# Kernel tuning notes

Hardware: AMD Instinct MI355X
Metric: run time of the kernel (lower is better)

Reference implementation:

```python
import jax, jax.numpy as jnp
import numpy as np

B, N, D, H, HID, EN = 2, 4096, 128, 4, 32, 16
ALPHA = 0.2           # LeakyReLU slope
NEG = -9e15           # masked_fill value from the original code


def setup_inputs() -> dict:
    key = jax.random.key(0)
    ks = jax.random.split(key, 6)
    fea = jax.random.normal(ks[0], (B, N, D), dtype=jnp.float32)
    # binary dense adjacency (regulon x gene), square here so narrow() is identity
    adj = jax.random.randint(ks[1], (B, N, N), 0, 2).astype(jnp.float32)
    # per-head GAT params (xavier-ish scale)
    W_heads = jax.random.normal(ks[2], (H, D, HID), dtype=jnp.float32) * 0.1
    a_heads = jax.random.normal(ks[3], (H, 2 * HID, 1), dtype=jnp.float32) * 0.1
    W_last = jax.random.normal(ks[4], (H * HID, EN), dtype=jnp.float32) * 0.1
    a_last = jax.random.normal(ks[5], (2 * EN, 1), dtype=jnp.float32) * 0.1
    return {"fea_mats": fea, "adj_mats": adj, "W_heads": W_heads,
            "a_heads": a_heads, "W_last": W_last, "a_last": a_last}


def _gat_layer(x, adj, W, a, concat):
    # x: [N, d_in], adj: [nr, N], W: [d_in, out], a: [2*out, 1]
    out_dim = W.shape[1]
    wh = x @ W                                   # [N, out]
    nr = adj.shape[0]
    wh1 = wh[:nr] @ a[:out_dim]                  # [nr, 1]
    wh2 = wh @ a[out_dim:]                       # [N, 1]
    e = jax.nn.leaky_relu(wh1 + wh2.T, ALPHA)    # [nr, N]
    # _prepare_attentions: mask by adj, weight by adj, fill zeros with -9e15
    att = jnp.where(adj != 0, e * adj, 0.0)
    att = jnp.where(att == 0, NEG, att)
    att = jax.nn.softmax(att, axis=1)
    # the original detaches attention via a numpy roundtrip
    att = jax.lax.stop_gradient(att)
    res = att @ wh                               # [nr, out]
    return jax.nn.elu(res) if concat else res


def reference(fea_mats, adj_mats, W_heads, a_heads, W_last, a_last):
    def per_sample(x, adj):
        # multi-head attention layers (concat=True), vmapped over heads
        heads = jax.vmap(lambda W, a: _gat_layer(x, adj, W, a, True))(W_heads, a_heads)  # [H, N, HID]
        xcat = jnp.transpose(heads, (1, 0, 2)).reshape(x.shape[0], H * HID)  # torch.cat(dim=1)
        nr = adj.shape[0]
        out = _gat_layer(xcat, adj[:, :nr], W_last, a_last, False)  # adj.narrow(1,0,nr)
        return jax.nn.elu(out)  # [N, EN]
    return jax.vmap(per_sample)(fea_mats, adj_mats)  # [B, N, EN]
```

## Files before the change

### kernel.cpp

```cpp
#include <hip/hip_runtime.h>
#include <hip/hip_bf16.h>
#include <stdint.h>

#define B_ 2
#define N_ 4096
#define D_ 128
#define H_ 4
#define HID_ 32
#define EN_ 16
#define ALPHA_ 0.2f
#define S1_ 4
#define S2_ 4
#define LOG2E_ 1.4426950408889634f

typedef __attribute__((ext_vector_type(8))) short bf16x8;
typedef __attribute__((ext_vector_type(4))) float f32x4;
typedef __attribute__((ext_vector_type(8))) unsigned short u16x8;

__device__ __forceinline__ float bf2f(unsigned short u) {
    return __uint_as_float(((unsigned int)u) << 16);
}
__device__ __forceinline__ unsigned short f2bf_rne(float x) {
    unsigned int u = __float_as_uint(x);
    unsigned int r = ((u >> 16) & 1u) + 0x7fffu;
    return (unsigned short)((u + r) >> 16);
}
__device__ __forceinline__ unsigned int f2key(float x) {
    unsigned int u = __float_as_uint(x);
    return (u & 0x80000000u) ? ~u : (u | 0x80000000u);
}
__device__ __forceinline__ float key2f(unsigned int k) {
    unsigned int u = (k & 0x80000000u) ? (k ^ 0x80000000u) : ~k;
    return __uint_as_float(u);
}

__global__ __launch_bounds__(256) void proj1_kernel(
    const float* __restrict__ fea, const float* __restrict__ Wh,
    float* __restrict__ wh)
{
    __shared__ float Ws[D_ * HID_];
    __shared__ float xs[8][D_];
    const int b = blockIdx.z, h = blockIdx.y;
    const int i0 = blockIdx.x * 8;
    const int tid = threadIdx.x;
    const float* Wp = Wh + h * D_ * HID_;
    for (int idx = tid * 4; idx < D_ * HID_; idx += 1024)
        *(float4*)&Ws[idx] = *(const float4*)(Wp + idx);
    const float* xp = fea + ((size_t)b * N_ + i0) * D_;
    *(float4*)&xs[(tid * 4) >> 7][(tid * 4) & 127] = *(const float4*)(xp + tid * 4);
    __syncthreads();
    const int r = tid >> 5, d = tid & 31;
    float acc = 0.f;
#pragma unroll 8
    for (int k = 0; k < D_; ++k) acc += xs[r][k] * Ws[k * HID_ + d];
    wh[(((size_t)b * H_ + h) * N_ + i0 + r) * HID_ + d] = acc;
}

__global__ __launch_bounds__(128) void proj1b_kernel(
    const float* __restrict__ wh, const float* __restrict__ a_heads,
    float* __restrict__ wh1, float* __restrict__ wh2,
    unsigned int* __restrict__ mkey, unsigned short* __restrict__ whTt)
{
    __shared__ float as_[2 * HID_];
    __shared__ unsigned short ts[32][136];
    const int b = blockIdx.z, h = blockIdx.y, tid = threadIdx.x;
    const int i = blockIdx.x * 128 + tid;
    if (tid < 2 * HID_) as_[tid] = a_heads[h * 2 * HID_ + tid];
    __syncthreads();
    const float* row = wh + (((size_t)b * H_ + h) * N_ + i) * HID_;
    float rv[32];
#pragma unroll
    for (int q = 0; q < 8; ++q) *(float4*)&rv[q * 4] = ((const float4*)row)[q];
    float a1 = 0.f, a2 = 0.f;
#pragma unroll
    for (int d = 0; d < HID_; ++d) {
        float v = rv[d];
        a1 += v * as_[d]; a2 += v * as_[HID_ + d];
        ts[d][tid] = f2bf_rne(v);
    }
    a1 *= LOG2E_; a2 *= LOG2E_;
    const size_t o = (size_t)(b * H_ + h) * N_ + i;
    wh1[o] = a1; wh2[o] = a2;
    float m = a2;
#pragma unroll
    for (int off = 32; off; off >>= 1) m = fmaxf(m, __shfl_xor(m, off));
    if ((tid & 63) == 0) atomicMax(&mkey[b * H_ + h], f2key(m));
    __syncthreads();
    const size_t base = ((size_t)(b * H_ + h) * 64 + blockIdx.x * 2) * 2048;
#pragma unroll
    for (int r = 0; r < 4; ++r) {
        int l = r * 128 + tid;
        int jb = l >> 8, d = (l >> 3) & 31, part = l & 7;
        *(u16x8*)(whTt + base + (size_t)jb * 2048 + d * 64 + part * 8) =
            *(const u16x8*)&ts[d][jb * 64 + part * 8];
    }
}

__global__ __launch_bounds__(256) void attn1_kernel(
    const float* __restrict__ adj, const unsigned short* __restrict__ whT,
    const float* __restrict__ wh1, const float* __restrict__ wh2,
    const unsigned int* __restrict__ mkey,
    float* __restrict__ x2num, float* __restrict__ l1sum)
{
    __shared__ float adj_s[2][16][68];
    const int b = blockIdx.z, split = blockIdx.y, i0 = blockIdx.x * 16;
    const int tid = threadIdx.x, lane = tid & 63, h = tid >> 6;
    const int m = lane & 15, quad = lane >> 4;
    const float w1r = wh1[(size_t)(b * H_ + h) * N_ + i0 + m];
    const float Mh = key2f(mkey[b * H_ + h]);
    const float sbound = w1r + Mh;
    const float mr = fmaxf(sbound, ALPHA_ * sbound);
    const float* adjb = adj + ((size_t)b * N_ + i0) * N_;
    const float* w2h = wh2 + (size_t)(b * H_ + h) * N_;
    const unsigned short* whTp = whT + (size_t)(b * H_ + h) * 64 * 2048;
    const int sr = tid >> 4, sc4 = (tid & 15) * 4;
    f32x4 acc0 = {0.f, 0.f, 0.f, 0.f}, acc1 = {0.f, 0.f, 0.f, 0.f};
    float lsum = 0.f;
    const int TL = N_ / S1_ / 64;
    const int jt0 = split * (N_ / S1_);

    auto stage = [&](int jt, int bufi) {
        *(float4*)&adj_s[bufi][sr][sc4] = *(const float4*)(adjb + (size_t)sr * N_ + jt + sc4);
    };
    stage(jt0, 0);
    int buf = 0;
    for (int t = 0; t < TL; ++t) {
        __syncthreads();
        if (t + 1 < TL) stage(jt0 + (t + 1) * 64, buf ^ 1);
        const int jt = jt0 + t * 64;
        const int jb = split * TL + t;
#pragma unroll
        for (int ks = 0; ks < 2; ++ks) {
            const int ko = ks * 32 + quad * 8;
            float av[8], wv8[8];
            *(float4*)&av[0] = *(const float4*)&adj_s[buf][m][ko];
            *(float4*)&av[4] = *(const float4*)&adj_s[buf][m][ko + 4];
            *(float4*)&wv8[0] = *(const float4*)(w2h + jt + ko);
            *(float4*)&wv8[4] = *(const float4*)(w2h + jt + ko + 4);
            bf16x8 af;
#pragma unroll
            for (int jj = 0; jj < 8; ++jj) {
                float s = w1r + wv8[jj];
                float e = fmaxf(s, ALPHA_ * s);
                float tt = (av[jj] == 0.f || s == 0.f) ? -__builtin_inff() : (e - mr);
                float p = __builtin_amdgcn_exp2f(tt);
                unsigned short pb = f2bf_rne(p);
                af[jj] = (short)pb;
                lsum += bf2f(pb);
            }
            const unsigned short* bp = whTp + (size_t)jb * 2048 + m * 64 + ks * 32 + quad * 8;
            bf16x8 b0 = *(const bf16x8*)bp;
            bf16x8 b1 = *(const bf16x8*)(bp + 1024);
            acc0 = __builtin_amdgcn_mfma_f32_16x16x32_bf16(af, b0, acc0, 0, 0, 0);
            acc1 = __builtin_amdgcn_mfma_f32_16x16x32_bf16(af, b1, acc1, 0, 0, 0);
        }
        buf ^= 1;
    }
#pragma unroll
    for (int reg = 0; reg < 4; ++reg) {
        int row = quad * 4 + reg;
        float* dst = x2num + ((size_t)b * N_ + i0 + row) * (H_ * HID_) + h * HID_;
        atomicAdd(dst + m, acc0[reg]);
        atomicAdd(dst + 16 + m, acc1[reg]);
    }
    lsum += __shfl_xor(lsum, 16);
    lsum += __shfl_xor(lsum, 32);
    if (quad == 0) atomicAdd(l1sum + ((size_t)b * N_ + i0 + m) * H_ + h, lsum);
}

__global__ __launch_bounds__(256) void proj2_kernel(
    const float* __restrict__ x2num, const float* __restrict__ l1sum,
    const float* __restrict__ Wl, float* __restrict__ whl2)
{
    __shared__ float Ws[D_ * EN_];
    __shared__ float xs[16][D_];
    const int b = blockIdx.y, i0 = blockIdx.x * 16, tid = threadIdx.x;
    for (int idx = tid * 4; idx < D_ * EN_; idx += 1024)
        *(float4*)&Ws[idx] = *(const float4*)(Wl + idx);
    for (int idx = tid * 4; idx < 16 * D_; idx += 1024) {
        int r = idx >> 7, hd = idx & 127, h = hd >> 5;
        const size_t i = (size_t)b * N_ + i0 + r;
        float linv = 1.f / fmaxf(l1sum[i * H_ + h], 1e-30f);
        float4 v = *(const float4*)(x2num + i * D_ + hd);
        float o0 = v.x * linv, o1 = v.y * linv, o2 = v.z * linv, o3 = v.w * linv;
        xs[r][hd]     = o0 > 0.f ? o0 : expm1f(o0);
        xs[r][hd + 1] = o1 > 0.f ? o1 : expm1f(o1);
        xs[r][hd + 2] = o2 > 0.f ? o2 : expm1f(o2);
        xs[r][hd + 3] = o3 > 0.f ? o3 : expm1f(o3);
    }
    __syncthreads();
    const int r = tid >> 4, e = tid & 15;
    float acc = 0.f;
#pragma unroll 8
    for (int k = 0; k < D_; ++k) acc += xs[r][k] * Ws[k * EN_ + e];
    whl2[((size_t)b * N_ + i0 + r) * EN_ + e] = acc;
}

__global__ __launch_bounds__(128) void proj2b_kernel(
    const float* __restrict__ whl2, const float* __restrict__ a_last,
    float* __restrict__ wh1b, float* __restrict__ wh2b,
    unsigned int* __restrict__ mkey2, unsigned short* __restrict__ whT2t)
{
    __shared__ float as_[2 * EN_];
    __shared__ unsigned short ts[16][136];
    const int b = blockIdx.y, tid = threadIdx.x;
    const int i = blockIdx.x * 128 + tid;
    if (tid < 2 * EN_) as_[tid] = a_last[tid];
    __syncthreads();
    const float* row = whl2 + ((size_t)b * N_ + i) * EN_;
    float rv[16];
#pragma unroll
    for (int q = 0; q < 4; ++q) *(float4*)&rv[q * 4] = ((const float4*)row)[q];
    float a1 = 0.f, a2 = 0.f;
#pragma unroll
    for (int e = 0; e < EN_; ++e) {
        float v = rv[e];
        a1 += v * as_[e]; a2 += v * as_[EN_ + e];
        ts[e][tid] = f2bf_rne(v);
    }
    a1 *= LOG2E_; a2 *= LOG2E_;
    wh1b[(size_t)b * N_ + i] = a1; wh2b[(size_t)b * N_ + i] = a2;
    float m = a2;
#pragma unroll
    for (int off = 32; off; off >>= 1) m = fmaxf(m, __shfl_xor(m, off));
    if ((tid & 63) == 0) atomicMax(mkey2 + b, f2key(m));
    __syncthreads();
    const size_t base = ((size_t)b * 64 + blockIdx.x * 2) * 1024;
#pragma unroll
    for (int r = 0; r < 2; ++r) {
        int l = r * 128 + tid;
        int jb = l >> 7, d = (l >> 3) & 15, part = l & 7;
        *(u16x8*)(whT2t + base + (size_t)jb * 1024 + d * 64 + part * 8) =
            *(const u16x8*)&ts[d][jb * 64 + part * 8];
    }
}

__global__ __launch_bounds__(256) void attn2_kernel(
    const float* __restrict__ adj, const unsigned short* __restrict__ whT2,
    const float* __restrict__ wh1b, const float* __restrict__ wh2b,
    const unsigned int* __restrict__ mkey2,
    float* __restrict__ out_num, float* __restrict__ out_l)
{
    __shared__ float adj_s[16][260];
    const int b = blockIdx.z, split = blockIdx.y, i0 = blockIdx.x * 16;
    const int tid = threadIdx.x, lane = tid & 63, wv = tid >> 6;
    const int m = lane & 15, quad = lane >> 4;
    const float w1r = wh1b[(size_t)b * N_ + i0 + m];
    const float Mh = key2f(mkey2[b]);
    const float sbound = w1r + Mh;
    const float mr = fmaxf(sbound, ALPHA_ * sbound);
    const float* adjb = adj + ((size_t)b * N_ + i0) * N_;
    const float* w2g = wh2b + (size_t)b * N_;
    const unsigned short* wTg = whT2 + (size_t)b * 64 * 1024;
    f32x4 acc = {0.f, 0.f, 0.f, 0.f};
    float lsum = 0.f;
    const int jt0 = split * (N_ / S2_);

    for (int bt = 0; bt < (N_ / S2_) / 256; ++bt) {
        const int jT = jt0 + bt * 256;
        __syncthreads();
#pragma unroll
        for (int r = 0; r < 4; ++r) {
            int l = r * 256 + tid;
            int row = l >> 6, c4 = (l & 63) * 4;
            *(float4*)&adj_s[row][c4] = *(const float4*)(adjb + (size_t)row * N_ + jT + c4);
        }
        __syncthreads();
        const int wbase = wv * 64;
        const int jb = split * 16 + bt * 4 + wv;
#pragma unroll
        for (int ks = 0; ks < 2; ++ks) {
            const int ko = wbase + ks * 32 + quad * 8;
            float av[8], wv8[8];
            *(float4*)&av[0] = *(const float4*)&adj_s[m][ko];
            *(float4*)&av[4] = *(const float4*)&adj_s[m][ko + 4];
            *(float4*)&wv8[0] = *(const float4*)(w2g + jT + ko);
            *(float4*)&wv8[4] = *(const float4*)(w2g + jT + ko + 4);
            bf16x8 af;
#pragma unroll
            for (int jj = 0; jj < 8; ++jj) {
                float s = w1r + wv8[jj];
                float e = fmaxf(s, ALPHA_ * s);
                float tt = (av[jj] == 0.f || s == 0.f) ? -__builtin_inff() : (e - mr);
                float p = __builtin_amdgcn_exp2f(tt);
                unsigned short pb = f2bf_rne(p);
                af[jj] = (short)pb;
                lsum += bf2f(pb);
            }
            bf16x8 b0 = *(const bf16x8*)(wTg + (size_t)jb * 1024 + m * 64 + ks * 32 + quad * 8);
            acc = __builtin_amdgcn_mfma_f32_16x16x32_bf16(af, b0, acc, 0, 0, 0);
        }
    }
#pragma unroll
    for (int reg = 0; reg < 4; ++reg) {
        int row = quad * 4 + reg;
        atomicAdd(out_num + ((size_t)b * N_ + i0 + row) * EN_ + m, acc[reg]);
    }
    lsum += __shfl_xor(lsum, 16);
    lsum += __shfl_xor(lsum, 32);
    if (quad == 0) atomicAdd(out_l + (size_t)b * N_ + i0 + m, lsum);
}

__global__ __launch_bounds__(256) void finalize2_kernel(
    const float* __restrict__ num, const float* __restrict__ l, float* __restrict__ out)
{
    const int id = blockIdx.x * 256 + threadIdx.x;
    float v = num[id] / fmaxf(l[id >> 4], 1e-30f);
    out[id] = v > 0.f ? v : expm1f(v);
}

extern "C" void kernel_launch(void* const* d_in, const int* in_sizes, int n_in,
                              void* d_out, int out_size, void* d_ws, size_t ws_size,
                              hipStream_t stream)
{
    const float* fea = (const float*)d_in[0];
    const float* adj = (const float*)d_in[1];
    const float* Wh  = (const float*)d_in[2];
    const float* ah  = (const float*)d_in[3];
    const float* Wl  = (const float*)d_in[4];
    const float* al  = (const float*)d_in[5];

    float* ws    = (float*)d_ws;
    float* wh    = ws;
    float* wh1   = wh   + (size_t)B_ * H_ * N_ * HID_;
    float* wh2   = wh1  + (size_t)B_ * H_ * N_;
    float* whl2  = wh2  + (size_t)B_ * H_ * N_;
    float* wh1b  = whl2 + (size_t)B_ * N_ * EN_;
    float* wh2b  = wh1b + (size_t)B_ * N_;
    float* x2num  = wh2b + (size_t)B_ * N_;
    float* l1sum  = x2num + (size_t)B_ * N_ * D_;
    float* outnum = l1sum + (size_t)B_ * N_ * H_;
    float* outl   = outnum + (size_t)B_ * N_ * EN_;
    unsigned int* mkey = (unsigned int*)(outl + (size_t)B_ * N_);
    size_t zero_bytes = ((size_t)B_ * N_ * (D_ + H_ + EN_ + 1)) * 4 + 64;
    unsigned short* whTt  = (unsigned short*)(mkey + 16);
    unsigned short* whT2t = whTt + (size_t)B_ * H_ * 64 * 2048;

    hipMemsetAsync(x2num, 0, zero_bytes, stream);
    proj1_kernel<<<dim3(N_ / 8, H_, B_), 256, 0, stream>>>(fea, Wh, wh);
    proj1b_kernel<<<dim3(N_ / 128, H_, B_), 128, 0, stream>>>(wh, ah, wh1, wh2, mkey, whTt);
    attn1_kernel<<<dim3(N_ / 16, S1_, B_), 256, 0, stream>>>(adj, whTt, wh1, wh2, mkey,
                                                             x2num, l1sum);
    proj2_kernel<<<dim3(N_ / 16, B_), 256, 0, stream>>>(x2num, l1sum, Wl, whl2);
    proj2b_kernel<<<dim3(N_ / 128, B_), 128, 0, stream>>>(whl2, al, wh1b, wh2b, mkey + 8, whT2t);
    attn2_kernel<<<dim3(N_ / 16, S2_, B_), 256, 0, stream>>>(adj, whT2t, wh1b, wh2b, mkey + 8,
                                                             outnum, outl);
    finalize2_kernel<<<(B_ * N_ * EN_) / 256, 256, 0, stream>>>(outnum, outl, (float*)d_out);
}
```

Baseline: 314.1 us.

## Compress adjacency to bitmask once, switch attention MMA to fp16, sum softmax via MFMA

A new kernel packs the fp32 adjacency into a one-bit-per-entry mask using wave ballots. Both attention kernels then read this small mask instead of streaming the full fp32 adjacency twice, which removes the adj shared-memory staging and its barriers. P and V operands move from bf16 with manual rounding to fp16 with packed RTZ conversion. The softmax denominator is now computed by an extra MFMA against a ones vector, replacing the scalar sum and shuffles. The mask pass still reads adj once, and fp16 changes the rounding and overflow behaviour of the attention weights and values.

```diff
diff --git a/kernel.cpp b/kernel.cpp
--- a/kernel.cpp
+++ b/kernel.cpp
@@ -13,18 +13,10 @@
 #define S2_ 4
 #define LOG2E_ 1.4426950408889634f
 
-typedef __attribute__((ext_vector_type(8))) short bf16x8;
+typedef __attribute__((ext_vector_type(8))) _Float16 f16x8;
 typedef __attribute__((ext_vector_type(4))) float f32x4;
 typedef __attribute__((ext_vector_type(8))) unsigned short u16x8;
 
-__device__ __forceinline__ float bf2f(unsigned short u) {
-    return __uint_as_float(((unsigned int)u) << 16);
-}
-__device__ __forceinline__ unsigned short f2bf_rne(float x) {
-    unsigned int u = __float_as_uint(x);
-    unsigned int r = ((u >> 16) & 1u) + 0x7fffu;
-    return (unsigned short)((u + r) >> 16);
-}
 __device__ __forceinline__ unsigned int f2key(float x) {
     unsigned int u = __float_as_uint(x);
     return (u & 0x80000000u) ? ~u : (u | 0x80000000u);
@@ -32,6 +24,33 @@
 __device__ __forceinline__ float key2f(unsigned int k) {
     unsigned int u = (k & 0x80000000u) ? (k ^ 0x80000000u) : ~k;
     return __uint_as_float(u);
+}
+__device__ __forceinline__ unsigned short f2h(float v) {
+    _Float16 h = (_Float16)v;
+    return *(unsigned short*)&h;
+}
+
+__global__ __launch_bounds__(256) void maskc_kernel(
+    const float* __restrict__ adj, unsigned long long* __restrict__ mask)
+{
+    const int b = blockIdx.y;
+    const int i = blockIdx.x * 4 + (threadIdx.x >> 6);
+    const int lane = threadIdx.x & 63;
+    const float* ar = adj + ((size_t)b * N_ + i) * N_;
+    unsigned long long* mrow = mask + ((size_t)b * N_ + i) * 64;
+    for (int w0 = 0; w0 < 16; ++w0) {
+        float v0 = ar[(w0 +  0) * 64 + lane];
+        float v1 = ar[(w0 + 16) * 64 + lane];
+        float v2 = ar[(w0 + 32) * 64 + lane];
+        float v3 = ar[(w0 + 48) * 64 + lane];
+        unsigned long long b0 = __ballot(v0 != 0.f);
+        unsigned long long b1 = __ballot(v1 != 0.f);
+        unsigned long long b2 = __ballot(v2 != 0.f);
+        unsigned long long b3 = __ballot(v3 != 0.f);
+        if (lane == 0) {
+            mrow[w0] = b0; mrow[w0 + 16] = b1; mrow[w0 + 32] = b2; mrow[w0 + 48] = b3;
+        }
+    }
 }
 
 __global__ __launch_bounds__(256) void proj1_kernel(
@@ -76,7 +95,7 @@
     for (int d = 0; d < HID_; ++d) {
         float v = rv[d];
         a1 += v * as_[d]; a2 += v * as_[HID_ + d];
-        ts[d][tid] = f2bf_rne(v);
+        ts[d][tid] = f2h(v);
     }
     a1 *= LOG2E_; a2 *= LOG2E_;
     const size_t o = (size_t)(b * H_ + h) * N_ + i;
@@ -97,64 +116,67 @@
 }
 
 __global__ __launch_bounds__(256) void attn1_kernel(
-    const float* __restrict__ adj, const unsigned short* __restrict__ whT,
+    const unsigned long long* __restrict__ mask, const unsigned short* __restrict__ whT,
     const float* __restrict__ wh1, const float* __restrict__ wh2,
     const unsigned int* __restrict__ mkey,
     float* __restrict__ x2num, float* __restrict__ l1sum)
 {
-    __shared__ float adj_s[2][16][68];
+    __shared__ unsigned long long mask_s[16][17];
     const int b = blockIdx.z, split = blockIdx.y, i0 = blockIdx.x * 16;
     const int tid = threadIdx.x, lane = tid & 63, h = tid >> 6;
     const int m = lane & 15, quad = lane >> 4;
+    mask_s[tid >> 4][tid & 15] =
+        mask[((size_t)b * N_ + i0 + (tid >> 4)) * 64 + split * 16 + (tid & 15)];
     const float w1r = wh1[(size_t)(b * H_ + h) * N_ + i0 + m];
     const float Mh = key2f(mkey[b * H_ + h]);
     const float sbound = w1r + Mh;
     const float mr = fmaxf(sbound, ALPHA_ * sbound);
-    const float* adjb = adj + ((size_t)b * N_ + i0) * N_;
     const float* w2h = wh2 + (size_t)(b * H_ + h) * N_;
     const unsigned short* whTp = whT + (size_t)(b * H_ + h) * 64 * 2048;
-    const int sr = tid >> 4, sc4 = (tid & 15) * 4;
     f32x4 acc0 = {0.f, 0.f, 0.f, 0.f}, acc1 = {0.f, 0.f, 0.f, 0.f};
-    float lsum = 0.f;
-    const int TL = N_ / S1_ / 64;
+    f32x4 acc2 = {0.f, 0.f, 0.f, 0.f};
+    f16x8 ones;
+#pragma unroll
+    for (int q = 0; q < 8; ++q) ones[q] = (_Float16)1.0f;
     const int jt0 = split * (N_ / S1_);
-
-    auto stage = [&](int jt, int bufi) {
-        *(float4*)&adj_s[bufi][sr][sc4] = *(const float4*)(adjb + (size_t)sr * N_ + jt + sc4);
-    };
-    stage(jt0, 0);
-    int buf = 0;
-    for (int t = 0; t < TL; ++t) {
-        __syncthreads();
-        if (t + 1 < TL) stage(jt0 + (t + 1) * 64, buf ^ 1);
+    __syncthreads();
+
+    for (int t = 0; t < N_ / S1_ / 64; ++t) {
         const int jt = jt0 + t * 64;
-        const int jb = split * TL + t;
+        const int jb = split * 16 + t;
+        unsigned long long wrd = mask_s[m][t];
+        unsigned int mh2[2] = {(unsigned int)wrd, (unsigned int)(wrd >> 32)};
 #pragma unroll
         for (int ks = 0; ks < 2; ++ks) {
             const int ko = ks * 32 + quad * 8;
-            float av[8], wv8[8];
-            *(float4*)&av[0] = *(const float4*)&adj_s[buf][m][ko];
-            *(float4*)&av[4] = *(const float4*)&adj_s[buf][m][ko + 4];
+            const unsigned int mby = mh2[ks];
+            float wv8[8];
             *(float4*)&wv8[0] = *(const float4*)(w2h + jt + ko);
             *(float4*)&wv8[4] = *(const float4*)(w2h + jt + ko + 4);
-            bf16x8 af;
-#pragma unroll
-            for (int jj = 0; jj < 8; ++jj) {
-                float s = w1r + wv8[jj];
-                float e = fmaxf(s, ALPHA_ * s);
-                float tt = (av[jj] == 0.f || s == 0.f) ? -__builtin_inff() : (e - mr);
-                float p = __builtin_amdgcn_exp2f(tt);
-                unsigned short pb = f2bf_rne(p);
-                af[jj] = (short)pb;
-                lsum += bf2f(pb);
+            f16x8 af;
+#pragma unroll
+            for (int q = 0; q < 4; ++q) {
+                float p2[2];
+#pragma unroll
+                for (int c = 0; c < 2; ++c) {
+                    int jj = q * 2 + c;
+                    float s = w1r + wv8[jj];
+                    float e = fmaxf(s, ALPHA_ * s);
+                    float tt = e - mr;
+                    unsigned int bit = (mby >> (quad * 8 + jj)) & 1u;
+                    tt = (bit == 0u || s == 0.f) ? -1e38f : tt;
+                    p2[c] = __builtin_amdgcn_exp2f(tt);
+                }
+                auto pr = __builtin_amdgcn_cvt_pkrtz(p2[0], p2[1]);
+                af[q * 2] = (_Float16)pr[0]; af[q * 2 + 1] = (_Float16)pr[1];
             }
             const unsigned short* bp = whTp + (size_t)jb * 2048 + m * 64 + ks * 32 + quad * 8;
-            bf16x8 b0 = *(const bf16x8*)bp;
-            bf16x8 b1 = *(const bf16x8*)(bp + 1024);
-            acc0 = __builtin_amdgcn_mfma_f32_16x16x32_bf16(af, b0, acc0, 0, 0, 0);
-            acc1 = __builtin_amdgcn_mfma_f32_16x16x32_bf16(af, b1, acc1, 0, 0, 0);
+            f16x8 b0 = *(const f16x8*)bp;
+            f16x8 b1 = *(const f16x8*)(bp + 1024);
+            acc0 = __builtin_amdgcn_mfma_f32_16x16x32_f16(af, b0, acc0, 0, 0, 0);
+            acc1 = __builtin_amdgcn_mfma_f32_16x16x32_f16(af, b1, acc1, 0, 0, 0);
+            acc2 = __builtin_amdgcn_mfma_f32_16x16x32_f16(af, ones, acc2, 0, 0, 0);
         }
-        buf ^= 1;
     }
 #pragma unroll
     for (int reg = 0; reg < 4; ++reg) {
@@ -162,10 +184,9 @@
         float* dst = x2num + ((size_t)b * N_ + i0 + row) * (H_ * HID_) + h * HID_;
         atomicAdd(dst + m, acc0[reg]);
         atomicAdd(dst + 16 + m, acc1[reg]);
-    }
-    lsum += __shfl_xor(lsum, 16);
-    lsum += __shfl_xor(lsum, 32);
-    if (quad == 0) atomicAdd(l1sum + ((size_t)b * N_ + i0 + m) * H_ + h, lsum);
+        if (m == 0)
+            atomicAdd(l1sum + ((size_t)b * N_ + i0 + row) * H_ + h, acc2[reg]);
+    }
 }
 
 __global__ __launch_bounds__(256) void proj2_kernel(
@@ -216,7 +237,7 @@
     for (int e = 0; e < EN_; ++e) {
         float v = rv[e];
         a1 += v * as_[e]; a2 += v * as_[EN_ + e];
-        ts[e][tid] = f2bf_rne(v);
+        ts[e][tid] = f2h(v);
     }
     a1 *= LOG2E_; a2 *= LOG2E_;
     wh1b[(size_t)b * N_ + i] = a1; wh2b[(size_t)b * N_ + i] = a2;
@@ -236,69 +257,73 @@
 }
 
 __global__ __launch_bounds__(256) void attn2_kernel(
-    const float* __restrict__ adj, const unsigned short* __restrict__ whT2,
+    const unsigned long long* __restrict__ mask, const unsigned short* __restrict__ whT2,
     const float* __restrict__ wh1b, const float* __restrict__ wh2b,
     const unsigned int* __restrict__ mkey2,
     float* __restrict__ out_num, float* __restrict__ out_l)
 {
-    __shared__ float adj_s[16][260];
+    __shared__ unsigned long long mask_s[16][17];
     const int b = blockIdx.z, split = blockIdx.y, i0 = blockIdx.x * 16;
     const int tid = threadIdx.x, lane = tid & 63, wv = tid >> 6;
     const int m = lane & 15, quad = lane >> 4;
+    mask_s[tid >> 4][tid & 15] =
+        mask[((size_t)b * N_ + i0 + (tid >> 4)) * 64 + split * 16 + (tid & 15)];
     const float w1r = wh1b[(size_t)b * N_ + i0 + m];
     const float Mh = key2f(mkey2[b]);
     const float sbound = w1r + Mh;
     const float mr = fmaxf(sbound, ALPHA_ * sbound);
-    const float* adjb = adj + ((size_t)b * N_ + i0) * N_;
     const float* w2g = wh2b + (size_t)b * N_;
     const unsigned short* wTg = whT2 + (size_t)b * 64 * 1024;
-    f32x4 acc = {0.f, 0.f, 0.f, 0.f};
-    float lsum = 0.f;
+    f32x4 acc = {0.f, 0.f, 0.f, 0.f}, acc2 = {0.f, 0.f, 0.f, 0.f};
+    f16x8 ones;
+#pragma unroll
+    for (int q = 0; q < 8; ++q) ones[q] = (_Float16)1.0f;
     const int jt0 = split * (N_ / S2_);
-
-    for (int bt = 0; bt < (N_ / S2_) / 256; ++bt) {
-        const int jT = jt0 + bt * 256;
-        __syncthreads();
-#pragma unroll
-        for (int r = 0; r < 4; ++r) {
-            int l = r * 256 + tid;
-            int row = l >> 6, c4 = (l & 63) * 4;
-            *(float4*)&adj_s[row][c4] = *(const float4*)(adjb + (size_t)row * N_ + jT + c4);
-        }
-        __syncthreads();
-        const int wbase = wv * 64;
-        const int jb = split * 16 + bt * 4 + wv;
+    __syncthreads();
+
+#pragma unroll
+    for (int t = 0; t < 4; ++t) {
+        const int tw = wv * 4 + t;
+        const int jt = jt0 + tw * 64;
+        const int jb = split * 16 + tw;
+        unsigned long long wrd = mask_s[m][tw];
+        unsigned int mh2[2] = {(unsigned int)wrd, (unsigned int)(wrd >> 32)};
 #pragma unroll
         for (int ks = 0; ks < 2; ++ks) {
-            const int ko = wbase + ks * 32 + quad * 8;
-            float av[8], wv8[8];
-            *(float4*)&av[0] = *(const float4*)&adj_s[m][ko];
-            *(float4*)&av[4] = *(const float4*)&adj_s[m][ko + 4];
-            *(float4*)&wv8[0] = *(const float4*)(w2g + jT + ko);
-            *(float4*)&wv8[4] = *(const float4*)(w2g + jT + ko + 4);
-            bf16x8 af;
-#pragma unroll
-            for (int jj = 0; jj < 8; ++jj) {
-                float s = w1r + wv8[jj];
-                float e = fmaxf(s, ALPHA_ * s);
-                float tt = (av[jj] == 0.f || s == 0.f) ? -__builtin_inff() : (e - mr);
-                float p = __builtin_amdgcn_exp2f(tt);
-                unsigned short pb = f2bf_rne(p);
-                af[jj] = (short)pb;
-                lsum += bf2f(pb);
+            const int ko = ks * 32 + quad * 8;
+            const unsigned int mby = mh2[ks];
+            float wv8[8];
+            *(float4*)&wv8[0] = *(const float4*)(w2g + jt + ko);
+            *(float4*)&wv8[4] = *(const float4*)(w2g + jt + ko + 4);
+            f16x8 af;
+#pragma unroll
+            for (int q = 0; q < 4; ++q) {
+                float p2[2];
+#pragma unroll
+                for (int c = 0; c < 2; ++c) {
+                    int jj = q * 2 + c;
+                    float s = w1r + wv8[jj];
+                    float e = fmaxf(s, ALPHA_ * s);
+                    float tt = e - mr;
+                    unsigned int bit = (mby >> (quad * 8 + jj)) & 1u;
+                    tt = (bit == 0u || s == 0.f) ? -1e38f : tt;
+                    p2[c] = __builtin_amdgcn_exp2f(tt);
+                }
+                auto pr = __builtin_amdgcn_cvt_pkrtz(p2[0], p2[1]);
+                af[q * 2] = (_Float16)pr[0]; af[q * 2 + 1] = (_Float16)pr[1];
             }
-            bf16x8 b0 = *(const bf16x8*)(wTg + (size_t)jb * 1024 + m * 64 + ks * 32 + quad * 8);
-            acc = __builtin_amdgcn_mfma_f32_16x16x32_bf16(af, b0, acc, 0, 0, 0);
+            f16x8 b0 = *(const f16x8*)(wTg + (size_t)jb * 1024 + m * 64 + ks * 32 + quad * 8);
+            acc = __builtin_amdgcn_mfma_f32_16x16x32_f16(af, b0, acc, 0, 0, 0);
+            acc2 = __builtin_amdgcn_mfma_f32_16x16x32_f16(af, ones, acc2, 0, 0, 0);
         }
     }
 #pragma unroll
     for (int reg = 0; reg < 4; ++reg) {
         int row = quad * 4 + reg;
         atomicAdd(out_num + ((size_t)b * N_ + i0 + row) * EN_ + m, acc[reg]);
-    }
-    lsum += __shfl_xor(lsum, 16);
-    lsum += __shfl_xor(lsum, 32);
-    if (quad == 0) atomicAdd(out_l + (size_t)b * N_ + i0 + m, lsum);
+        if (m == 0)
+            atomicAdd(out_l + (size_t)b * N_ + i0 + row, acc2[reg]);
+    }
 }
 
 __global__ __launch_bounds__(256) void finalize2_kernel(
@@ -335,15 +360,18 @@
     size_t zero_bytes = ((size_t)B_ * N_ * (D_ + H_ + EN_ + 1)) * 4 + 64;
     unsigned short* whTt  = (unsigned short*)(mkey + 16);
     unsigned short* whT2t = whTt + (size_t)B_ * H_ * 64 * 2048;
+    unsigned long long* mask =
+        (unsigned long long*)(whT2t + (size_t)B_ * 64 * 1024);
 
     hipMemsetAsync(x2num, 0, zero_bytes, stream);
+    maskc_kernel<<<dim3(N_ / 4, B_), 256, 0, stream>>>(adj, mask);
     proj1_kernel<<<dim3(N_ / 8, H_, B_), 256, 0, stream>>>(fea, Wh, wh);
     proj1b_kernel<<<dim3(N_ / 128, H_, B_), 128, 0, stream>>>(wh, ah, wh1, wh2, mkey, whTt);
-    attn1_kernel<<<dim3(N_ / 16, S1_, B_), 256, 0, stream>>>(adj, whTt, wh1, wh2, mkey,
+    attn1_kernel<<<dim3(N_ / 16, S1_, B_), 256, 0, stream>>>(mask, whTt, wh1, wh2, mkey,
                                                              x2num, l1sum);
     proj2_kernel<<<dim3(N_ / 16, B_), 256, 0, stream>>>(x2num, l1sum, Wl, whl2);
     proj2b_kernel<<<dim3(N_ / 128, B_), 128, 0, stream>>>(whl2, al, wh1b, wh2b, mkey + 8, whT2t);
-    attn2_kernel<<<dim3(N_ / 16, S2_, B_), 256, 0, stream>>>(adj, whT2t, wh1b, wh2b, mkey + 8,
+    attn2_kernel<<<dim3(N_ / 16, S2_, B_), 256, 0, stream>>>(mask, whT2t, wh1b, wh2b, mkey + 8,
                                                              outnum, outl);
     finalize2_kernel<<<(B_ * N_ * EN_) / 256, 256, 0, stream>>>(outnum, outl, (float*)d_out);
 }
```

New measurement: 358.3 us. +14.1%, slower.
